# Kernel optimization log

Measured on AMD Instinct MI355X. Metric: run time of the kernel, lower is better.

## Reference

```python
import jax, jax.numpy as jnp
import numpy as np

D_MODEL = 1024
N_HEAD = 16
B, S = 4, 1024


def _linear(x, W, b):
    # torch nn.Linear: y = x @ W.T + b, W: [out, in]
    return jnp.einsum('bsd,ed->bse', x, W) + b


def _split(x):
    b, s, d = x.shape
    return x.reshape(b, s, N_HEAD, d // N_HEAD).transpose(0, 2, 1, 3)  # [b,h,s,dh]


def _concat(x):
    b, h, s, dh = x.shape
    return x.transpose(0, 2, 1, 3).reshape(b, s, h * dh)


def _attention(q, k, v):
    dh = q.shape[-1]
    scale = 1.0 / np.float32(np.sqrt(dh))
    scores = jnp.einsum('bhqd,bhkd->bhqk', q, k) * scale
    probs = jax.nn.softmax(scores, axis=-1)
    return jnp.einsum('bhqk,bhkd->bhqd', probs, v)


def setup_inputs() -> dict:
    key = jax.random.key(0)
    ks = jax.random.split(key, 20)
    sc = 1.0 / np.float32(np.sqrt(D_MODEL))
    inp = {
        'q': jax.random.normal(ks[0], (B, S, D_MODEL), jnp.float32),
        'k': jax.random.normal(ks[1], (B, S, D_MODEL), jnp.float32),
        'v': jax.random.normal(ks[2], (B, S, D_MODEL), jnp.float32),
    }
    names = ['Wq', 'Wk', 'Wv', 'Wq2', 'Wk2', 'Wv2', 'Wc', 'Wc2']
    for i, n in enumerate(names):
        inp[n] = jax.random.normal(ks[3 + i], (D_MODEL, D_MODEL), jnp.float32) * sc
        inp['b' + n[1:]] = jnp.zeros((D_MODEL,), jnp.float32)
    return inp


def reference(q, k, v, Wq, bq, Wk, bk, Wv, bv, Wq2, bq2, Wk2, bk2, Wv2, bv2, Wc, bc, Wc2, bc2):
    # path 1 projections
    q1 = _linear(q, Wq, bq)
    k1 = _linear(k, Wk, bk)
    v1 = _linear(v, Wv, bv)
    # path 2 projections (note cross-wiring: q2 from k, k2/v2 from q)
    q2 = _linear(k, Wq2, bq2)
    k2 = _linear(q, Wk2, bk2)
    v2 = _linear(q, Wv2, bv2)

    out1 = _attention(_split(q1), _split(k1), _split(v1))
    out2 = _attention(_split(q2), _split(k2), _split(v2))

    out1 = _linear(_concat(out1), Wc, bc)
    out2 = _linear(_concat(out2), Wc2, bc2)
    return out1, out2
```

## Files before the change

### kernel.cpp

```cpp
#include <hip/hip_runtime.h>
#include <hip/hip_bf16.h>

#define B_ 4
#define S_ 1024
#define D_ 1024
#define H_ 16
#define M_ 4096

typedef unsigned short u16;
typedef __attribute__((ext_vector_type(4))) float f32x4;
typedef __attribute__((ext_vector_type(16))) float f32x16;
typedef __attribute__((ext_vector_type(8))) short short8;
typedef __attribute__((ext_vector_type(4))) u16 u16x4;

__device__ inline u16 f2bf(float f) {
  return __builtin_bit_cast(u16, __float2bfloat16(f));
}

__device__ inline short8 ldfrag(const u16* p) {
  return *reinterpret_cast<const short8*>(p);
}

__device__ inline void gload_lds16(const void* g, void* l) {
  __builtin_amdgcn_global_load_lds((const __attribute__((address_space(1))) void*)g,
                                   (__attribute__((address_space(3))) void*)l,
                                   16, 0, 0);
}

__device__ inline int sigma_s(int s) {
  return (s & ~12) | ((s & 4) << 1) | ((s & 8) >> 1);
}

struct GArgs {
  const void* A[6];
  const void* W[6];
  const float* bias[6];
  void* C[6];
  float oscale[6];
  int vtrans[6];
};

struct CvtArgs {
  const float* src[11];
  u16* dst[11];
  int n4[11];
};

__global__ __launch_bounds__(256) void cvt_f32_bf16(CvtArgs a) {
  const int z = blockIdx.y;
  const float4* s = (const float4*)a.src[z];
  u16x4* d = (u16x4*)a.dst[z];
  const int n4 = a.n4[z];
  for (int i = blockIdx.x * blockDim.x + threadIdx.x; i < n4; i += gridDim.x * blockDim.x) {
    float4 v = s[i];
    u16x4 o;
    o[0] = f2bf(v.x); o[1] = f2bf(v.y); o[2] = f2bf(v.z); o[3] = f2bf(v.w);
    d[i] = o;
  }
}

template<typename CT>
__global__ __launch_bounds__(512, 2) void gemm_bt_256(GArgs args) {
  const int z = blockIdx.z;
  const u16* A = (const u16*)args.A[z];
  const u16* W = (const u16*)args.W[z];
  const float* bias = args.bias[z];
  CT* C = (CT*)args.C[z];
  const float oscale = args.oscale[z];
  const int vtrans = args.vtrans[z];

  __shared__ u16 AB[2][2][256 * 64];

  const int tid = threadIdx.x;
  const int lane = tid & 63;
  const int w = tid >> 6;
  const int wm = w >> 2, wn = w & 3;
  const int l15 = lane & 15, lhi = lane >> 4;

  const int lin = blockIdx.x + blockIdx.y * 4;
  const int xcd = lin & 7, idx = lin >> 3;
  const int by = xcd * 2 + (idx >> 2), bx = idx & 3;
  const int m0 = by * 256, n0 = bx * 256;

  const int srow = tid >> 3;
  const int scol = (((tid & 7) ^ ((tid >> 3) & 7)) << 3);

  f32x4 acc[8][4];
#pragma unroll
  for (int m = 0; m < 8; ++m)
#pragma unroll
    for (int n = 0; n < 4; ++n) acc[m][n] = f32x4{0.f, 0.f, 0.f, 0.f};

  {
    const u16* Ag = A + (size_t)m0 * 1024;
    const u16* Wg = W + (size_t)n0 * 1024;
#pragma unroll
    for (int i = 0; i < 4; ++i) {
      gload_lds16(Ag + (size_t)(i * 64 + srow) * 1024 + scol, &AB[0][0][i * 4096 + w * 512]);
      gload_lds16(Wg + (size_t)(i * 64 + srow) * 1024 + scol, &AB[0][1][i * 4096 + w * 512]);
    }
  }

  for (int t = 0; t < 16; ++t) {
    const int db = t & 1;

    asm volatile("s_waitcnt vmcnt(0)" ::: "memory");
    __builtin_amdgcn_s_barrier();
    __builtin_amdgcn_sched_barrier(0);

    if (t < 15) {
      const u16* Ag = A + (size_t)m0 * 1024 + (t + 1) * 64;
      const u16* Wg = W + (size_t)n0 * 1024 + (t + 1) * 64;
#pragma unroll
      for (int i = 0; i < 4; ++i) {
        gload_lds16(Ag + (size_t)(i * 64 + srow) * 1024 + scol, &AB[db ^ 1][0][i * 4096 + w * 512]);
        gload_lds16(Wg + (size_t)(i * 64 + srow) * 1024 + scol, &AB[db ^ 1][1][i * 4096 + w * 512]);
      }
    }

#pragma unroll
    for (int kk = 0; kk < 2; ++kk) {
      short8 af[8], bf4[4];
#pragma unroll
      for (int m = 0; m < 8; ++m) {
        int row = wm * 128 + m * 16 + l15;
        af[m] = ldfrag(&AB[db][0][row * 64 + ((kk * 32 + lhi * 8) ^ ((l15 & 7) << 3))]);
      }
#pragma unroll
      for (int n = 0; n < 4; ++n) {
        int row = wn * 64 + n * 16 + l15;
        bf4[n] = ldfrag(&AB[db][1][row * 64 + ((kk * 32 + lhi * 8) ^ ((l15 & 7) << 3))]);
      }
      __builtin_amdgcn_s_setprio(1);
#pragma unroll
      for (int m = 0; m < 8; ++m)
#pragma unroll
        for (int n = 0; n < 4; ++n)
          acc[m][n] = __builtin_amdgcn_mfma_f32_16x16x32_bf16(af[m], bf4[n], acc[m][n], 0, 0, 0);
      __builtin_amdgcn_s_setprio(0);
    }
  }

#pragma unroll
  for (int m = 0; m < 8; ++m) {
#pragma unroll
    for (int n = 0; n < 4; ++n) {
      int ncol = n0 + wn * 64 + n * 16 + l15;
      float bsv = bias[ncol];
      int mb = m0 + wm * 128 + m * 16 + lhi * 4;
      if (vtrans) {
        int h = ncol >> 6, d = ncol & 63;
        int b = mb >> 10, s0 = sigma_s(mb & 1023);
        u16x4 ov;
#pragma unroll
        for (int r = 0; r < 4; ++r) ov[r] = f2bf((acc[m][n][r] + bsv) * oscale);
        *reinterpret_cast<u16x4*>((u16*)C + ((size_t)((b * 16 + h) * 64 + d)) * 1024 + s0) = ov;
      } else {
#pragma unroll
        for (int r = 0; r < 4; ++r) {
          float val = (acc[m][n][r] + bsv) * oscale;
          if constexpr (sizeof(CT) == 2) ((u16*)C)[(size_t)(mb + r) * 1024 + ncol] = f2bf(val);
          else ((float*)C)[(size_t)(mb + r) * 1024 + ncol] = val;
        }
      }
    }
  }
}

template<typename CT>
__global__ __launch_bounds__(256) void gemm_bt_lds(GArgs args) {
  const int z = blockIdx.z;
  const u16* A = (const u16*)args.A[z];
  const u16* W = (const u16*)args.W[z];
  const float* bias = args.bias[z];
  CT* C = (CT*)args.C[z];
  const float oscale = args.oscale[z];
  const int vtrans = args.vtrans[z];

  __shared__ u16 Al[128 * 64];
  __shared__ u16 Bl[128 * 64];

  const int tid = threadIdx.x;
  const int lane = tid & 63;
  const int w = tid >> 6;
  const int wr = w >> 1, wc = w & 1;
  const int l15 = lane & 15, lhi = lane >> 4;

  const int lin = blockIdx.x + blockIdx.y * 8;
  const int xcd = lin & 7, idx = lin >> 3;
  const int bx = (xcd & 1) * 4 + (idx >> 3);
  const int by = (xcd >> 1) * 8 + (idx & 7);
  const int m0 = by * 128, n0 = bx * 128;

  const int srow = lane >> 3;
  const int scol = (lane & 7) * 8;

  const f32x4 vzero = {0.f, 0.f, 0.f, 0.f};
  f32x4 acc[4][4];
#pragma unroll
  for (int i = 0; i < 4; ++i)
#pragma unroll
    for (int j = 0; j < 4; ++j) acc[i][j] = vzero;

  for (int kt = 0; kt < 1024; kt += 64) {
    __syncthreads();
    const u16* Ag = A + (size_t)m0 * 1024 + kt;
    const u16* Wg = W + (size_t)n0 * 1024 + kt;
#pragma unroll
    for (int j = 0; j < 4; ++j) {
      int rb = w * 32 + j * 8;
      gload_lds16(Ag + (size_t)(rb + srow) * 1024 + scol, &Al[rb * 64]);
      gload_lds16(Wg + (size_t)(rb + srow) * 1024 + scol, &Bl[rb * 64]);
    }
    __syncthreads();

#pragma unroll
    for (int c = 0; c < 2; ++c) {
      short8 af[4], bfr[4];
#pragma unroll
      for (int i = 0; i < 4; ++i) af[i] = ldfrag(&Al[(wr * 64 + i * 16 + l15) * 64 + c * 32 + lhi * 8]);
#pragma unroll
      for (int j = 0; j < 4; ++j) bfr[j] = ldfrag(&Bl[(wc * 64 + j * 16 + l15) * 64 + c * 32 + lhi * 8]);
#pragma unroll
      for (int i = 0; i < 4; ++i)
#pragma unroll
        for (int j = 0; j < 4; ++j)
          acc[i][j] = __builtin_amdgcn_mfma_f32_16x16x32_bf16(af[i], bfr[j], acc[i][j], 0, 0, 0);
    }
  }

#pragma unroll
  for (int i = 0; i < 4; ++i) {
#pragma unroll
    for (int j = 0; j < 4; ++j) {
      int n = n0 + wc * 64 + j * 16 + l15;
      float bsv = bias[n];
      int mb = m0 + wr * 64 + i * 16 + lhi * 4;
      if (vtrans) {
        int h = n >> 6, d = n & 63;
        int b = mb >> 10, s0 = sigma_s(mb & 1023);
        u16x4 ov;
#pragma unroll
        for (int r = 0; r < 4; ++r) ov[r] = f2bf((acc[i][j][r] + bsv) * oscale);
        *reinterpret_cast<u16x4*>((u16*)C + ((size_t)((b * 16 + h) * 64 + d)) * 1024 + s0) = ov;
      } else {
#pragma unroll
        for (int r = 0; r < 4; ++r) {
          float val = (acc[i][j][r] + bsv) * oscale;
          if constexpr (sizeof(CT) == 2) ((u16*)C)[(size_t)(mb + r) * 1024 + n] = f2bf(val);
          else ((float*)C)[(size_t)(mb + r) * 1024 + n] = val;
        }
      }
    }
  }
}

template<typename AT, typename CT>
__global__ __launch_bounds__(256) void gemm_bt_batched(GArgs args) {
  const int z = blockIdx.z;
  const AT* A = (const AT*)args.A[z];
  const float* W = (const float*)args.W[z];
  const float* bias = args.bias[z];
  CT* C = (CT*)args.C[z];
  const float oscale = args.oscale[z];
  const int vtrans = args.vtrans[z];

  __shared__ u16 Al[128][72];
  __shared__ u16 Bl[128][72];

  const int tid = threadIdx.x;
  const int lane = tid & 63;
  const int wid = tid >> 6;
  const int wr = wid >> 1, wc = wid & 1;
  const int m0 = blockIdx.y * 128, n0 = blockIdx.x * 128;
  const int l15 = lane & 15, lhi = lane >> 4;

  const f32x4 vzero = {0.f, 0.f, 0.f, 0.f};
  f32x4 acc[4][4];
#pragma unroll
  for (int i = 0; i < 4; ++i)
#pragma unroll
    for (int j = 0; j < 4; ++j) acc[i][j] = vzero;

  for (int kt = 0; kt < 1024; kt += 64) {
    __syncthreads();
#pragma unroll
    for (int i = 0; i < 8; ++i) {
      int g = tid + i * 256;
      int row = g >> 4, col = (g & 15) * 4;
      u16x4 bv;
      if constexpr (sizeof(AT) == 4) {
        float4 vv = *reinterpret_cast<const float4*>((const float*)A + (size_t)(m0 + row) * 1024 + kt + col);
        bv[0] = f2bf(vv.x); bv[1] = f2bf(vv.y); bv[2] = f2bf(vv.z); bv[3] = f2bf(vv.w);
      } else {
        bv = *reinterpret_cast<const u16x4*>((const u16*)A + (size_t)(m0 + row) * 1024 + kt + col);
      }
      *reinterpret_cast<u16x4*>(&Al[row][col]) = bv;
    }
#pragma unroll
    for (int i = 0; i < 8; ++i) {
      int g = tid + i * 256;
      int row = g >> 4, col = (g & 15) * 4;
      float4 vv = *reinterpret_cast<const float4*>((const float*)W + (size_t)(n0 + row) * 1024 + kt + col);
      u16x4 bv;
      bv[0] = f2bf(vv.x); bv[1] = f2bf(vv.y); bv[2] = f2bf(vv.z); bv[3] = f2bf(vv.w);
      *reinterpret_cast<u16x4*>(&Bl[row][col]) = bv;
    }
    __syncthreads();

#pragma unroll
    for (int c = 0; c < 2; ++c) {
      short8 af[4], bfr[4];
#pragma unroll
      for (int i = 0; i < 4; ++i) af[i] = ldfrag(&Al[wr * 64 + i * 16 + l15][c * 32 + lhi * 8]);
#pragma unroll
      for (int j = 0; j < 4; ++j) bfr[j] = ldfrag(&Bl[wc * 64 + j * 16 + l15][c * 32 + lhi * 8]);
#pragma unroll
      for (int i = 0; i < 4; ++i)
#pragma unroll
        for (int j = 0; j < 4; ++j)
          acc[i][j] = __builtin_amdgcn_mfma_f32_16x16x32_bf16(af[i], bfr[j], acc[i][j], 0, 0, 0);
    }
  }

#pragma unroll
  for (int i = 0; i < 4; ++i) {
#pragma unroll
    for (int j = 0; j < 4; ++j) {
      int n = n0 + wc * 64 + j * 16 + l15;
      float bsv = bias[n];
      int mb = m0 + wr * 64 + i * 16 + lhi * 4;
      if (vtrans) {
        int h = n >> 6, d = n & 63;
        int b = mb >> 10, s0 = sigma_s(mb & 1023);
        u16x4 ov;
#pragma unroll
        for (int r = 0; r < 4; ++r) ov[r] = f2bf((acc[i][j][r] + bsv) * oscale);
        *reinterpret_cast<u16x4*>((u16*)C + ((size_t)((b * 16 + h) * 64 + d)) * 1024 + s0) = ov;
      } else {
#pragma unroll
        for (int r = 0; r < 4; ++r) {
          float val = (acc[i][j][r] + bsv) * oscale;
          if constexpr (sizeof(CT) == 2) ((u16*)C)[(size_t)(mb + r) * 1024 + n] = f2bf(val);
          else ((float*)C)[(size_t)(mb + r) * 1024 + n] = val;
        }
      }
    }
  }
}

__global__ __launch_bounds__(256, 2) void attn_fused32b(const u16* q1b, const u16* k1b, const u16* vt1,
                                                        const u16* q2b, const u16* k2b, const u16* vt2,
                                                        u16* o1, u16* o2) {
  const int lin = blockIdx.x + blockIdx.y * 4;
  const int swz = (lin & 7) * 8 + (lin >> 3);
  const int qt = swz & 3;
  const int h = swz >> 2;
  const int zb = blockIdx.z;
  const int path = zb >> 2, b = zb & 3;

  const u16* Q = (path == 0) ? q1b : q2b;
  const u16* K = (path == 0) ? k1b : k2b;
  const u16* V = (path == 0) ? vt1 : vt2;
  u16* O = (path == 0) ? o1 : o2;

  const size_t base_qk = (size_t)b * S_ * D_ + (size_t)h * 64;
  const size_t vbase = (size_t)((b * 16 + h) * 64) * 1024;
  const int tid = threadIdx.x;
  const int lane = tid & 63, w = tid >> 6;
  const int lq = lane & 31, hi = lane >> 5;

  __shared__ u16 Ks[2][64][72];
  __shared__ u16 Vs[2][64][72];

  const int srow = tid >> 3;
  const int scol = (tid & 7) * 8;

  const int qbase_row = qt * 256 + w * 64;
  short8 qf[2][4];
#pragma unroll
  for (int qtile = 0; qtile < 2; ++qtile)
#pragma unroll
    for (int dhg = 0; dhg < 4; ++dhg)
      qf[qtile][dhg] = ldfrag(Q + base_qk + (size_t)(qbase_row + qtile * 32 + lq) * 1024 + dhg * 16 + hi * 8);

  f32x16 o_acc[2][2] = {};
  float m_r[2] = {-1e30f, -1e30f};
  float l_r[2] = {0.f, 0.f};

  {
    short8 r0 = ldfrag(K + base_qk + (size_t)srow * 1024 + scol);
    short8 r1 = ldfrag(K + base_qk + (size_t)(srow + 32) * 1024 + scol);
    short8 r2 = ldfrag(V + vbase + (size_t)srow * 1024 + scol);
    short8 r3 = ldfrag(V + vbase + (size_t)(srow + 32) * 1024 + scol);
    *reinterpret_cast<short8*>(&Ks[0][srow][scol]) = r0;
    *reinterpret_cast<short8*>(&Ks[0][srow + 32][scol]) = r1;
    *reinterpret_cast<short8*>(&Vs[0][srow][scol]) = r2;
    *reinterpret_cast<short8*>(&Vs[0][srow + 32][scol]) = r3;
  }
  __syncthreads();

  for (int kv = 0; kv < 16; ++kv) {
    const int cur = kv & 1;

    short8 n0, n1, n2, n3;
    if (kv < 15) {
      const u16* kg = K + base_qk + (size_t)((kv + 1) * 64) * 1024;
      const u16* vg = V + vbase + (kv + 1) * 64;
      n0 = ldfrag(kg + (size_t)srow * 1024 + scol);
      n1 = ldfrag(kg + (size_t)(srow + 32) * 1024 + scol);
      n2 = ldfrag(vg + (size_t)srow * 1024 + scol);
      n3 = ldfrag(vg + (size_t)(srow + 32) * 1024 + scol);
    }

    f32x16 s[2][2] = {};
    __builtin_amdgcn_s_setprio(1);
#pragma unroll
    for (int dhg = 0; dhg < 4; ++dhg) {
#pragma unroll
      for (int keytile = 0; keytile < 2; ++keytile) {
        short8 ka = ldfrag(&Ks[cur][keytile * 32 + lq][dhg * 16 + hi * 8]);
#pragma unroll
        for (int qtile = 0; qtile < 2; ++qtile)
          s[keytile][qtile] = __builtin_amdgcn_mfma_f32_32x32x16_bf16(ka, qf[qtile][dhg], s[keytile][qtile], 0, 0, 0);
      }
    }
    __builtin_amdgcn_s_setprio(0);

#pragma unroll
    for (int qtile = 0; qtile < 2; ++qtile) {
      float pm = s[0][qtile][0];
#pragma unroll
      for (int r = 1; r < 16; ++r) pm = fmaxf(pm, s[0][qtile][r]);
#pragma unroll
      for (int r = 0; r < 16; ++r) pm = fmaxf(pm, s[1][qtile][r]);
      pm = fmaxf(pm, __shfl_xor(pm, 32));

      if (!__all(pm <= m_r[qtile] + 8.f)) {
        float mn = fmaxf(m_r[qtile], pm);
        float sc = __expf(m_r[qtile] - mn);
        m_r[qtile] = mn;
        l_r[qtile] *= sc;
        o_acc[0][qtile] *= sc;
        o_acc[1][qtile] *= sc;
      }
      const float mn = m_r[qtile];
      float sum = 0.f;
#pragma unroll
      for (int kt = 0; kt < 2; ++kt)
#pragma unroll
        for (int r = 0; r < 16; ++r) {
          float e = __expf(s[kt][qtile][r] - mn);
          s[kt][qtile][r] = e;
          sum += e;
        }
      sum += __shfl_xor(sum, 32);
      l_r[qtile] += sum;
    }

    __builtin_amdgcn_s_setprio(1);
#pragma unroll
    for (int g = 0; g < 4; ++g) {
      short8 va0 = ldfrag(&Vs[cur][lq][g * 16 + hi * 8]);
      short8 va1 = ldfrag(&Vs[cur][32 + lq][g * 16 + hi * 8]);
#pragma unroll
      for (int qtile = 0; qtile < 2; ++qtile) {
        short8 pb;
#pragma unroll
        for (int j = 0; j < 8; ++j) {
          float pv = (g < 2) ? s[0][qtile][(g & 1) * 8 + j] : s[1][qtile][(g & 1) * 8 + j];
          pb[j] = (short)f2bf(pv);
        }
        o_acc[0][qtile] = __builtin_amdgcn_mfma_f32_32x32x16_bf16(va0, pb, o_acc[0][qtile], 0, 0, 0);
        o_acc[1][qtile] = __builtin_amdgcn_mfma_f32_32x32x16_bf16(va1, pb, o_acc[1][qtile], 0, 0, 0);
      }
    }
    __builtin_amdgcn_s_setprio(0);

    __syncthreads();
    if (kv < 15) {
      const int nxt = cur ^ 1;
      *reinterpret_cast<short8*>(&Ks[nxt][srow][scol]) = n0;
      *reinterpret_cast<short8*>(&Ks[nxt][srow + 32][scol]) = n1;
      *reinterpret_cast<short8*>(&Vs[nxt][srow][scol]) = n2;
      *reinterpret_cast<short8*>(&Vs[nxt][srow + 32][scol]) = n3;
      __syncthreads();
    }
  }

#pragma unroll
  for (int qtile = 0; qtile < 2; ++qtile) {
    float inv = 1.0f / l_r[qtile];
    u16* Op = O + base_qk + (size_t)(qbase_row + qtile * 32 + lq) * 1024;
#pragma unroll
    for (int dtile = 0; dtile < 2; ++dtile) {
#pragma unroll
      for (int qd = 0; qd < 4; ++qd) {
        u16x4 ov;
#pragma unroll
        for (int r = 0; r < 4; ++r) ov[r] = f2bf(o_acc[dtile][qtile][qd * 4 + r] * inv);
        *reinterpret_cast<u16x4*>(Op + dtile * 32 + 8 * qd + 4 * hi) = ov;
      }
    }
  }
}

extern "C" void kernel_launch(void* const* d_in, const int* in_sizes, int n_in,
                              void* d_out, int out_size, void* d_ws, size_t ws_size,
                              hipStream_t stream) {
  const float* q   = (const float*)d_in[0];
  const float* k   = (const float*)d_in[1];
  const float* v   = (const float*)d_in[2];
  const float* Wq  = (const float*)d_in[3];  const float* bq  = (const float*)d_in[4];
  const float* Wk  = (const float*)d_in[5];  const float* bk  = (const float*)d_in[6];
  const float* Wv  = (const float*)d_in[7];  const float* bv  = (const float*)d_in[8];
  const float* Wq2 = (const float*)d_in[9];  const float* bq2 = (const float*)d_in[10];
  const float* Wk2 = (const float*)d_in[11]; const float* bk2 = (const float*)d_in[12];
  const float* Wv2 = (const float*)d_in[13]; const float* bv2 = (const float*)d_in[14];
  const float* Wc  = (const float*)d_in[15]; const float* bc  = (const float*)d_in[16];
  const float* Wc2 = (const float*)d_in[17]; const float* bc2 = (const float*)d_in[18];

  u16* ws = (u16*)d_ws;
  const size_t SZ = (size_t)M_ * D_;
  const size_t WSZ = (size_t)D_ * D_;
  u16* q1b = ws + 0 * SZ;
  u16* k1b = ws + 1 * SZ;
  u16* vt1 = ws + 2 * SZ;
  u16* q2b = ws + 3 * SZ;
  u16* k2b = ws + 4 * SZ;
  u16* vt2 = ws + 5 * SZ;
  u16* a1  = ws + 6 * SZ;
  u16* a2  = ws + 7 * SZ;

  const size_t need = (11 * SZ + 8 * WSZ) * sizeof(u16);

  if (ws_size >= need) {
    u16* qb = ws + 8 * SZ;
    u16* kb = ws + 9 * SZ;
    u16* vb = ws + 10 * SZ;
    u16* wbase = ws + 11 * SZ;
    u16* WqB  = wbase + 0 * WSZ;
    u16* WkB  = wbase + 1 * WSZ;
    u16* WvB  = wbase + 2 * WSZ;
    u16* Wq2B = wbase + 3 * WSZ;
    u16* Wk2B = wbase + 4 * WSZ;
    u16* Wv2B = wbase + 5 * WSZ;
    u16* WcB  = wbase + 6 * WSZ;
    u16* Wc2B = wbase + 7 * WSZ;

    CvtArgs ca;
    ca.src[0] = q;   ca.dst[0] = qb;   ca.n4[0] = (int)(SZ / 4);
    ca.src[1] = k;   ca.dst[1] = kb;   ca.n4[1] = (int)(SZ / 4);
    ca.src[2] = v;   ca.dst[2] = vb;   ca.n4[2] = (int)(SZ / 4);
    ca.src[3] = Wq;  ca.dst[3] = WqB;  ca.n4[3] = (int)(WSZ / 4);
    ca.src[4] = Wk;  ca.dst[4] = WkB;  ca.n4[4] = (int)(WSZ / 4);
    ca.src[5] = Wv;  ca.dst[5] = WvB;  ca.n4[5] = (int)(WSZ / 4);
    ca.src[6] = Wq2; ca.dst[6] = Wq2B; ca.n4[6] = (int)(WSZ / 4);
    ca.src[7] = Wk2; ca.dst[7] = Wk2B; ca.n4[7] = (int)(WSZ / 4);
    ca.src[8] = Wv2; ca.dst[8] = Wv2B; ca.n4[8] = (int)(WSZ / 4);
    ca.src[9] = Wc;  ca.dst[9] = WcB;  ca.n4[9] = (int)(WSZ / 4);
    ca.src[10] = Wc2; ca.dst[10] = Wc2B; ca.n4[10] = (int)(WSZ / 4);
    cvt_f32_bf16<<<dim3(512, 11), dim3(256), 0, stream>>>(ca);

    GArgs pa;
    pa.A[0] = qb; pa.W[0] = WqB;  pa.bias[0] = bq;  pa.C[0] = q1b; pa.oscale[0] = 0.125f; pa.vtrans[0] = 0;
    pa.A[1] = kb; pa.W[1] = WkB;  pa.bias[1] = bk;  pa.C[1] = k1b; pa.oscale[1] = 1.0f;   pa.vtrans[1] = 0;
    pa.A[2] = vb; pa.W[2] = WvB;  pa.bias[2] = bv;  pa.C[2] = vt1; pa.oscale[2] = 1.0f;   pa.vtrans[2] = 1;
    pa.A[3] = kb; pa.W[3] = Wq2B; pa.bias[3] = bq2; pa.C[3] = q2b; pa.oscale[3] = 0.125f; pa.vtrans[3] = 0;
    pa.A[4] = qb; pa.W[4] = Wk2B; pa.bias[4] = bk2; pa.C[4] = k2b; pa.oscale[4] = 1.0f;   pa.vtrans[4] = 0;
    pa.A[5] = qb; pa.W[5] = Wv2B; pa.bias[5] = bv2; pa.C[5] = vt2; pa.oscale[5] = 1.0f;   pa.vtrans[5] = 1;
    gemm_bt_256<u16><<<dim3(4, 16, 6), dim3(512), 0, stream>>>(pa);

    attn_fused32b<<<dim3(4, 16, 8), dim3(256), 0, stream>>>(q1b, k1b, vt1, q2b, k2b, vt2, a1, a2);

    GArgs fa;
    fa.A[0] = a1; fa.W[0] = WcB;  fa.bias[0] = bc;  fa.C[0] = (float*)d_out;      fa.oscale[0] = 1.0f; fa.vtrans[0] = 0;
    fa.A[1] = a2; fa.W[1] = Wc2B; fa.bias[1] = bc2; fa.C[1] = (float*)d_out + SZ; fa.oscale[1] = 1.0f; fa.vtrans[1] = 0;
    gemm_bt_lds<float><<<dim3(8, 32, 2), dim3(256), 0, stream>>>(fa);
  } else {
    GArgs pa;
    pa.A[0] = q; pa.W[0] = Wq;  pa.bias[0] = bq;  pa.C[0] = q1b; pa.oscale[0] = 0.125f; pa.vtrans[0] = 0;
    pa.A[1] = k; pa.W[1] = Wk;  pa.bias[1] = bk;  pa.C[1] = k1b; pa.oscale[1] = 1.0f;   pa.vtrans[1] = 0;
    pa.A[2] = v; pa.W[2] = Wv;  pa.bias[2] = bv;  pa.C[2] = vt1; pa.oscale[2] = 1.0f;   pa.vtrans[2] = 1;
    pa.A[3] = k; pa.W[3] = Wq2; pa.bias[3] = bq2; pa.C[3] = q2b; pa.oscale[3] = 0.125f; pa.vtrans[3] = 0;
    pa.A[4] = q; pa.W[4] = Wk2; pa.bias[4] = bk2; pa.C[4] = k2b; pa.oscale[4] = 1.0f;   pa.vtrans[4] = 0;
    pa.A[5] = q; pa.W[5] = Wv2; pa.bias[5] = bv2; pa.C[5] = vt2; pa.oscale[5] = 1.0f;   pa.vtrans[5] = 1;
    gemm_bt_batched<float, u16><<<dim3(8, 32, 6), dim3(256), 0, stream>>>(pa);

    attn_fused32b<<<dim3(4, 16, 8), dim3(256), 0, stream>>>(q1b, k1b, vt1, q2b, k2b, vt2, a1, a2);

    GArgs fa;
    fa.A[0] = a1; fa.W[0] = Wc;  fa.bias[0] = bc;  fa.C[0] = (float*)d_out;      fa.oscale[0] = 1.0f; fa.vtrans[0] = 0;
    fa.A[1] = a2; fa.W[1] = Wc2; fa.bias[1] = bc2; fa.C[1] = (float*)d_out + SZ; fa.oscale[1] = 1.0f; fa.vtrans[1] = 0;
    gemm_bt_batched<u16, float><<<dim3(8, 32, 2), dim3(256), 0, stream>>>(fa);
  }
}
```

Baseline: 166.9 us.

## Double-buffer output-projection GEMM with XOR-swizzled LDS and prefetch

Replaces the single-buffered output-projection GEMM with a double-buffered version that issues the global-to-LDS loads for the next k-tile while the current tile's MFMAs run, using one barrier per iteration instead of two. It also XOR-swizzles the LDS column layout to reduce bank conflicts on fragment reads, and raises MFMA wave priority. The cost is twice the LDS (64KB per block), which may limit occupancy despite the launch bound of 2.

```diff
diff --git a/kernel.cpp b/kernel.cpp
--- a/kernel.cpp
+++ b/kernel.cpp
@@ -168,7 +168,7 @@
 }
 
 template<typename CT>
-__global__ __launch_bounds__(256) void gemm_bt_lds(GArgs args) {
+__global__ __launch_bounds__(256, 2) void gemm_128db(GArgs args) {
   const int z = blockIdx.z;
   const u16* A = (const u16*)args.A[z];
   const u16* W = (const u16*)args.W[z];
@@ -177,8 +177,7 @@
   const float oscale = args.oscale[z];
   const int vtrans = args.vtrans[z];
 
-  __shared__ u16 Al[128 * 64];
-  __shared__ u16 Bl[128 * 64];
+  __shared__ u16 AB[2][2][128 * 64];
 
   const int tid = threadIdx.x;
   const int lane = tid & 63;
@@ -192,63 +191,82 @@
   const int by = (xcd >> 1) * 8 + (idx & 7);
   const int m0 = by * 128, n0 = bx * 128;
 
-  const int srow = lane >> 3;
-  const int scol = (lane & 7) * 8;
-
-  const f32x4 vzero = {0.f, 0.f, 0.f, 0.f};
+  const int srow = tid >> 3;
+  const int scol = (((tid & 7) ^ ((tid >> 3) & 7)) << 3);
+
   f32x4 acc[4][4];
 #pragma unroll
-  for (int i = 0; i < 4; ++i)
-#pragma unroll
-    for (int j = 0; j < 4; ++j) acc[i][j] = vzero;
-
-  for (int kt = 0; kt < 1024; kt += 64) {
-    __syncthreads();
-    const u16* Ag = A + (size_t)m0 * 1024 + kt;
-    const u16* Wg = W + (size_t)n0 * 1024 + kt;
-#pragma unroll
-    for (int j = 0; j < 4; ++j) {
-      int rb = w * 32 + j * 8;
-      gload_lds16(Ag + (size_t)(rb + srow) * 1024 + scol, &Al[rb * 64]);
-      gload_lds16(Wg + (size_t)(rb + srow) * 1024 + scol, &Bl[rb * 64]);
-    }
-    __syncthreads();
-
-#pragma unroll
-    for (int c = 0; c < 2; ++c) {
-      short8 af[4], bfr[4];
-#pragma unroll
-      for (int i = 0; i < 4; ++i) af[i] = ldfrag(&Al[(wr * 64 + i * 16 + l15) * 64 + c * 32 + lhi * 8]);
-#pragma unroll
-      for (int j = 0; j < 4; ++j) bfr[j] = ldfrag(&Bl[(wc * 64 + j * 16 + l15) * 64 + c * 32 + lhi * 8]);
-#pragma unroll
-      for (int i = 0; i < 4; ++i)
-#pragma unroll
-        for (int j = 0; j < 4; ++j)
-          acc[i][j] = __builtin_amdgcn_mfma_f32_16x16x32_bf16(af[i], bfr[j], acc[i][j], 0, 0, 0);
-    }
-  }
-
-#pragma unroll
-  for (int i = 0; i < 4; ++i) {
-#pragma unroll
-    for (int j = 0; j < 4; ++j) {
-      int n = n0 + wc * 64 + j * 16 + l15;
-      float bsv = bias[n];
-      int mb = m0 + wr * 64 + i * 16 + lhi * 4;
+  for (int m = 0; m < 4; ++m)
+#pragma unroll
+    for (int n = 0; n < 4; ++n) acc[m][n] = f32x4{0.f, 0.f, 0.f, 0.f};
+
+  const u16* Abase = A + (size_t)m0 * 1024;
+  const u16* Wbase = W + (size_t)n0 * 1024;
+
+  auto stage = [&](int kt, int r) {
+    const u16* Ag = Abase + kt * 64;
+    const u16* Wg = Wbase + kt * 64;
+#pragma unroll
+    for (int i = 0; i < 4; ++i) {
+      gload_lds16(Ag + (size_t)(i * 32 + srow) * 1024 + scol, &AB[r][0][i * 2048 + w * 512]);
+      gload_lds16(Wg + (size_t)(i * 32 + srow) * 1024 + scol, &AB[r][1][i * 2048 + w * 512]);
+    }
+  };
+
+  stage(0, 0);
+
+  for (int t = 0; t < 16; ++t) {
+    const int db = t & 1;
+
+    asm volatile("s_waitcnt vmcnt(0)" ::: "memory");
+    __builtin_amdgcn_s_barrier();
+    __builtin_amdgcn_sched_barrier(0);
+
+    if (t < 15) stage(t + 1, db ^ 1);
+
+#pragma unroll
+    for (int kk = 0; kk < 2; ++kk) {
+      short8 af[4], bf[4];
+#pragma unroll
+      for (int m = 0; m < 4; ++m) {
+        int row = wr * 64 + m * 16 + l15;
+        af[m] = ldfrag(&AB[db][0][row * 64 + ((kk * 32 + lhi * 8) ^ ((l15 & 7) << 3))]);
+      }
+#pragma unroll
+      for (int n = 0; n < 4; ++n) {
+        int row = wc * 64 + n * 16 + l15;
+        bf[n] = ldfrag(&AB[db][1][row * 64 + ((kk * 32 + lhi * 8) ^ ((l15 & 7) << 3))]);
+      }
+      __builtin_amdgcn_s_setprio(1);
+#pragma unroll
+      for (int m = 0; m < 4; ++m)
+#pragma unroll
+        for (int n = 0; n < 4; ++n)
+          acc[m][n] = __builtin_amdgcn_mfma_f32_16x16x32_bf16(af[m], bf[n], acc[m][n], 0, 0, 0);
+      __builtin_amdgcn_s_setprio(0);
+    }
+  }
+
+#pragma unroll
+  for (int m = 0; m < 4; ++m) {
+#pragma unroll
+    for (int n = 0; n < 4; ++n) {
+      int ncol = n0 + wc * 64 + n * 16 + l15;
+      float bsv = bias[ncol];
+      int mb = m0 + wr * 64 + m * 16 + lhi * 4;
       if (vtrans) {
-        int h = n >> 6, d = n & 63;
+        int h = ncol >> 6, d = ncol & 63;
         int b = mb >> 10, s0 = sigma_s(mb & 1023);
         u16x4 ov;
 #pragma unroll
-        for (int r = 0; r < 4; ++r) ov[r] = f2bf((acc[i][j][r] + bsv) * oscale);
+        for (int r = 0; r < 4; ++r) ov[r] = f2bf((acc[m][n][r] + bsv) * oscale);
         *reinterpret_cast<u16x4*>((u16*)C + ((size_t)((b * 16 + h) * 64 + d)) * 1024 + s0) = ov;
       } else {
 #pragma unroll
         for (int r = 0; r < 4; ++r) {
-          float val = (acc[i][j][r] + bsv) * oscale;
-          if constexpr (sizeof(CT) == 2) ((u16*)C)[(size_t)(mb + r) * 1024 + n] = f2bf(val);
-          else ((float*)C)[(size_t)(mb + r) * 1024 + n] = val;
+          float val = (acc[m][n][r] + bsv) * oscale;
+          if constexpr (sizeof(CT) == 2) ((u16*)C)[(size_t)(mb + r) * 1024 + ncol] = f2bf(val);
+          else ((float*)C)[(size_t)(mb + r) * 1024 + ncol] = val;
         }
       }
     }
@@ -576,7 +594,7 @@
     GArgs fa;
     fa.A[0] = a1; fa.W[0] = WcB;  fa.bias[0] = bc;  fa.C[0] = (float*)d_out;      fa.oscale[0] = 1.0f; fa.vtrans[0] = 0;
     fa.A[1] = a2; fa.W[1] = Wc2B; fa.bias[1] = bc2; fa.C[1] = (float*)d_out + SZ; fa.oscale[1] = 1.0f; fa.vtrans[1] = 0;
-    gemm_bt_lds<float><<<dim3(8, 32, 2), dim3(256), 0, stream>>>(fa);
+    gemm_128db<float><<<dim3(8, 32, 2), dim3(256), 0, stream>>>(fa);
   } else {
     GArgs pa;
     pa.A[0] = q; pa.W[0] = Wq;  pa.bias[0] = bq;  pa.C[0] = q1b; pa.oscale[0] = 0.125f; pa.vtrans[0] = 0;
```

Result: faster. 160.0 us (-4.2%).
